# Performance work log

Measured on AMD Instinct MI355X. Metric: run time of the kernel, lower is better.

Reference implementation:

```python
import jax, jax.numpy as jnp
import numpy as np
import math

B, T, D, E, K, H = 2, 2048, 1024, 8, 2, 4096
CAP_F = 1.25
N = B * T
C = math.ceil(CAP_F * N * K / E)  # 1280


def setup_inputs() -> dict:
    key = jax.random.key(0)
    ks = jax.random.split(key, 4)
    s = 0.02
    return {
        "h": jax.random.normal(ks[0], (B, T, D), jnp.float32),
        "Wr": (jax.random.normal(ks[1], (D, E), jnp.float32) * s),
        "br": jnp.zeros((E,), jnp.float32),
        "ln_scale": jnp.ones((E, D), jnp.float32),
        "ln_bias": jnp.zeros((E, D), jnp.float32),
        "W1": (jax.random.normal(ks[2], (E, D, 2 * H), jnp.float32) * s),
        "b1": jnp.zeros((E, 2 * H), jnp.float32),
        "W2": (jax.random.normal(ks[3], (E, H, D), jnp.float32) * s),
        "b2": jnp.zeros((E, D), jnp.float32),
    }


def _cv_squared(x, eps=1e-9):
    m = x.mean()
    v = ((x - m) ** 2).mean()  # biased variance, as torch var(unbiased=False)
    return v / (jnp.maximum(m, eps) ** 2 + eps)


def reference(h, Wr, br, ln_scale, ln_bias, W1, b1, W2, b2):
    x = h.reshape(N, D)
    # ---- router (eval mode: no noise, temperature=1.0) ----
    logits = x @ Wr + br                                   # [N, E]
    z_loss = jnp.mean(logits ** 2) * 1e-4
    probs = jax.nn.softmax(logits, axis=-1)
    importance = probs.sum(0)                              # [E]
    topk_vals, topk_idx = jax.lax.top_k(logits, K)         # [N, K]
    gates = jax.nn.softmax(topk_vals, axis=-1)             # [N, K]

    # ---- capacity-limited positions, pass-major order (pass 0 all tokens, then pass 1) ----
    eid = topk_idx.T.reshape(-1)                           # [K*N] int
    onehot = jax.nn.one_hot(eid, E, dtype=jnp.int32)       # [K*N, E]
    pos = jnp.take_along_axis(jnp.cumsum(onehot, 0) - 1, eid[:, None], axis=1)[:, 0]
    keep = pos < C                                         # [K*N] bool
    load = jnp.sum(onehot * keep[:, None].astype(jnp.int32), axis=0).astype(jnp.float32)
    pos_c = jnp.minimum(pos, C - 1)
    nid = jnp.tile(jnp.arange(N), K)                       # token ids, pass-major

    # normalized combine weights per token (dropped slots get 0)
    keep_nk = keep.reshape(K, N).T                         # [N, K]
    kept_gates = gates * keep_nk.astype(gates.dtype)
    denom = jnp.maximum(kept_gates.sum(1, keepdims=True), 1e-8)
    w_flat = (kept_gates / denom).T.reshape(-1)            # [K*N], pass-major

    # ---- dispatch: scatter tokens into [E, C, D] (== einsum('nec,nd->ecd')) ----
    keep_f = keep[:, None].astype(x.dtype)
    expert_in = jnp.zeros((E, C, D), x.dtype).at[eid, pos_c].add(x[nid] * keep_f)

    # ---- experts: PreNorm + GLU FFN (dropout off in eval) ----
    mu = expert_in.mean(-1, keepdims=True)
    var = ((expert_in - mu) ** 2).mean(-1, keepdims=True)
    xn = (expert_in - mu) / jnp.sqrt(var + 1e-5)
    xn = xn * ln_scale[:, None, :] + ln_bias[:, None, :]
    u = jnp.einsum('ecd,edh->ech', xn, W1) + b1[:, None, :]  # [E, C, 2H]
    a, g = u[..., :H], u[..., H:]
    v = a * jax.nn.sigmoid(g)                               # GLU(dim=-1)
    expert_out = jnp.einsum('ech,ehd->ecd', v, W2) + b2[:, None, :]

    # ---- combine: gather expert slots, weight, scatter-add to tokens ----
    gathered = expert_out[eid, pos_c] * w_flat[:, None]
    y = jnp.zeros((N, D), x.dtype).at[nid].add(gathered).reshape(B, T, D)

    balance_loss = 0.5 * (_cv_squared(importance) + _cv_squared(load))
    return y, balance_loss, z_loss
```

## Files before the change

### kernel.cpp

```cpp
#include <hip/hip_runtime.h>
#include <cstdint>
#include <cstddef>

#define N_TOK 4096
#define DIM   1024
#define NEXP  8
#define HID   4096
#define TWO_H 8192
#define CAP   1280

typedef __bf16 bf16x8 __attribute__((ext_vector_type(8)));
typedef float  f32x4  __attribute__((ext_vector_type(4)));

__device__ __forceinline__ unsigned short f2bf(float f) {
  union { float f; unsigned u; } v; v.f = f;
  unsigned r = v.u + 0x7FFF + ((v.u >> 16) & 1);
  return (unsigned short)(r >> 16);
}
__device__ __forceinline__ float bf2f(unsigned short b) {
  union { unsigned u; float f; } v; v.u = ((unsigned)b) << 16;
  return v.f;
}

__global__ void k_zero(float* imp, float* zsum) {
  if (threadIdx.x < NEXP) imp[threadIdx.x] = 0.f;
  if (threadIdx.x == 0) zsum[0] = 0.f;
}

__global__ void k_conv_w1(const float* __restrict__ W1, unsigned short* __restrict__ W1t) {
  __shared__ float tA[32][33];
  __shared__ float tG[32][33];
  int h0 = blockIdx.x * 32, d0 = blockIdx.y * 32, e = blockIdx.z;
  int tx = threadIdx.x & 31, ty = threadIdx.x >> 5;
  const float* src = W1 + (size_t)e * DIM * TWO_H;
  for (int i = 0; i < 32; i += 8) {
    int d = d0 + ty + i;
    tA[ty + i][tx] = src[(size_t)d * TWO_H + h0 + tx];
    tG[ty + i][tx] = src[(size_t)d * TWO_H + HID + h0 + tx];
  }
  __syncthreads();
  unsigned short* dst = W1t + (size_t)e * TWO_H * DIM;
  for (int i = 0; i < 64; i += 8) {
    int r = ty + i;
    int hh = r >> 1, p = r & 1;
    float v = p ? tG[tx][hh] : tA[tx][hh];
    dst[(size_t)(2 * h0 + r) * DIM + d0 + tx] = f2bf(v);
  }
}

__global__ void k_conv_w2(const float* __restrict__ W2, unsigned short* __restrict__ W2t) {
  __shared__ float t[32][33];
  int d0 = blockIdx.x * 32, h0 = blockIdx.y * 32, e = blockIdx.z;
  int tx = threadIdx.x & 31, ty = threadIdx.x >> 5;
  const float* src = W2 + (size_t)e * HID * DIM;
  for (int i = 0; i < 32; i += 8)
    t[ty + i][tx] = src[(size_t)(h0 + ty + i) * DIM + d0 + tx];
  __syncthreads();
  unsigned short* dst = W2t + (size_t)e * DIM * HID;
  for (int i = 0; i < 32; i += 8)
    dst[(size_t)(d0 + ty + i) * HID + h0 + tx] = f2bf(t[tx][ty + i]);
}

__global__ void k_pack_b1(const float* __restrict__ b1, float* __restrict__ b1p) {
  int g = blockIdx.x * blockDim.x + threadIdx.x;
  int e = g >> 13, r = g & (TWO_H - 1);
  int h = r >> 1, p = r & 1;
  b1p[g] = b1[e * TWO_H + p * HID + h];
}

__global__ void __launch_bounds__(256) k_router(
    const float* __restrict__ x, const float* __restrict__ Wr, const float* __restrict__ br,
    int* __restrict__ idx, float* __restrict__ gate,
    float* __restrict__ imp, float* __restrict__ zsum) {
  __shared__ float sW[TWO_H];
  __shared__ float sX[16 * 1028];
  __shared__ float sLG[16 * 8];
  __shared__ float sImp[8];
  __shared__ float sZ;
  int tid = threadIdx.x;
  if (tid < 8) sImp[tid] = 0.f;
  if (tid == 8) sZ = 0.f;
  for (int i = 0; i < 8; ++i) {
    int g = tid + i * 256;
    *(float4*)&sW[g * 4] = *(const float4*)&Wr[g * 4];
  }
  int t0 = blockIdx.x * 16;
  const float* xb = x + (size_t)t0 * DIM;
  for (int i = 0; i < 16; ++i) {
    int g = tid + i * 256;
    int row = g >> 8, c = (g & 255) * 4;
    *(float4*)&sX[row * 1028 + c] = *(const float4*)&xb[(size_t)g * 4];
  }
  __syncthreads();
  int t = tid >> 4, e = (tid >> 1) & 7, half = tid & 1;
  const float* xr = &sX[t * 1028 + half * 512];
  float s = 0.f;
  for (int k = 0; k < 512; k += 4) {
    float4 xv = *(const float4*)&xr[k];
    int kb = (half * 512 + k) * 8 + e;
    s += xv.x * sW[kb] + xv.y * sW[kb + 8] + xv.z * sW[kb + 16] + xv.w * sW[kb + 24];
  }
  s += __shfl_xor(s, 1);
  if (half == 0) sLG[t * 8 + e] = s + br[e];
  __syncthreads();
  if (tid < 16) {
    int n = t0 + tid;
    float lg[8];
    for (int i = 0; i < 8; ++i) lg[i] = sLG[tid * 8 + i];
    float mx = lg[0];
    for (int i = 1; i < 8; ++i) mx = fmaxf(mx, lg[i]);
    float ex[8], den = 0.f, zs = 0.f;
    for (int i = 0; i < 8; ++i) { ex[i] = __expf(lg[i] - mx); den += ex[i]; zs += lg[i] * lg[i]; }
    atomicAdd(&sZ, zs);
    float rden = 1.f / den;
    for (int i = 0; i < 8; ++i) atomicAdd(&sImp[i], ex[i] * rden);
    int i1 = 0;
    for (int i = 1; i < 8; ++i) if (lg[i] > lg[i1]) i1 = i;
    int i2 = -1;
    for (int i = 0; i < 8; ++i) { if (i == i1) continue; if (i2 < 0 || lg[i] > lg[i2]) i2 = i; }
    float e2 = __expf(lg[i2] - lg[i1]);
    float g1 = 1.f / (1.f + e2);
    idx[n * 2] = i1; idx[n * 2 + 1] = i2;
    gate[n * 2] = g1; gate[n * 2 + 1] = 1.f - g1;
  }
  __syncthreads();
  if (tid < 8) atomicAdd(&imp[tid], sImp[tid]);
  if (tid == 8) atomicAdd(zsum, sZ);
}

__global__ void k_scan(const int* __restrict__ idx, int* __restrict__ pos, int* __restrict__ cnt) {
  int wave = threadIdx.x >> 6, lane = threadIdx.x & 63;
  int base = 0;
  for (int c = 0; c < (2 * N_TOK) / 64; ++c) {
    int s = c * 64 + lane;
    int n = s & (N_TOK - 1), k = s >> 12;
    int e = idx[n * 2 + k];
    unsigned long long m = __ballot(e == wave);
    if (e == wave) pos[s] = base + __popcll(m & ((1ull << lane) - 1ull));
    base += __popcll(m);
  }
  if (lane == 0) cnt[wave] = base;
}

__global__ void k_weights(const float* __restrict__ gate, const int* __restrict__ pos,
                          float* __restrict__ wn) {
  int n = blockIdx.x * blockDim.x + threadIdx.x;
  if (n >= N_TOK) return;
  float g0 = gate[n * 2], g1 = gate[n * 2 + 1];
  float k0 = (pos[n] < CAP) ? g0 : 0.f;
  float k1 = (pos[N_TOK + n] < CAP) ? g1 : 0.f;
  float den = fmaxf(k0 + k1, 1e-8f);
  wn[n * 2] = k0 / den; wn[n * 2 + 1] = k1 / den;
}

__global__ void __launch_bounds__(256) k_gather_ln(
    const float* __restrict__ x, const float* __restrict__ lns, const float* __restrict__ lnb,
    const int* __restrict__ idx, const int* __restrict__ pos, unsigned short* __restrict__ Xn) {
  int s = blockIdx.x;
  int p = pos[s];
  if (p >= CAP) return;
  int n = s & (N_TOK - 1), k = s >> 12;
  int e = idx[n * 2 + k];
  const float* xr = x + (size_t)n * DIM;
  int tid = threadIdx.x;
  float v[4], sum = 0.f, sq = 0.f;
  for (int i = 0; i < 4; ++i) { v[i] = xr[tid + i * 256]; sum += v[i]; sq += v[i] * v[i]; }
  for (int o = 32; o > 0; o >>= 1) { sum += __shfl_down(sum, o); sq += __shfl_down(sq, o); }
  __shared__ float ws[8];
  int wv = tid >> 6, ln = tid & 63;
  if (ln == 0) { ws[wv] = sum; ws[4 + wv] = sq; }
  __syncthreads();
  sum = ws[0] + ws[1] + ws[2] + ws[3];
  sq  = ws[4] + ws[5] + ws[6] + ws[7];
  float mu = sum * (1.f / DIM);
  float var = sq * (1.f / DIM) - mu * mu;
  float rs = rsqrtf(var + 1e-5f);
  unsigned short* orow = Xn + ((size_t)e * CAP + p) * DIM;
  const float* sc = lns + (size_t)e * DIM;
  const float* bi = lnb + (size_t)e * DIM;
  for (int i = 0; i < 4; ++i) {
    int d = tid + i * 256;
    orow[d] = f2bf((v[i] - mu) * rs * sc[d] + bi[d]);
  }
}

template<bool GLU>
__global__ void __launch_bounds__(256) k_gemm(
    const unsigned short* __restrict__ A,
    const unsigned short* __restrict__ B,
    const float* __restrict__ bias,
    unsigned short* __restrict__ Cout,
    int M, int Nn, int K) {
  __shared__ __align__(16) unsigned short smem[2 * 128 * 72];
  unsigned short* sA = smem;
  unsigned short* sB = smem + 128 * 72;
  int e  = blockIdx.z;
  int m0 = blockIdx.x * 128;
  int n0 = blockIdx.y * 128;
  const unsigned short* Ae = A + (size_t)e * M * K;
  const unsigned short* Be = B + (size_t)e * Nn * K;
  int tid = threadIdx.x;
  int lane = tid & 63, wave = tid >> 6;
  int wm = (wave >> 1) * 64, wn = (wave & 1) * 64;
  int quad = lane >> 4, l16 = lane & 15;
  f32x4 acc[4][4];
  for (int i = 0; i < 4; ++i)
    for (int j = 0; j < 4; ++j) acc[i][j] = f32x4{0.f, 0.f, 0.f, 0.f};

  int srow = tid >> 3;
  int schunk = (tid & 7) * 8;
  for (int k0 = 0; k0 < K; k0 += 64) {
    __syncthreads();
    for (int i = 0; i < 4; ++i) {
      int r = srow + i * 32;
      *(int4*)&sA[r * 72 + schunk] = *(const int4*)&Ae[(size_t)(m0 + r) * K + k0 + schunk];
      *(int4*)&sB[r * 72 + schunk] = *(const int4*)&Be[(size_t)(n0 + r) * K + k0 + schunk];
    }
    __syncthreads();
    for (int kk = 0; kk < 64; kk += 32) {
      bf16x8 aF[4], bF[4];
      for (int i = 0; i < 4; ++i) {
        aF[i] = *(const bf16x8*)&sA[(wm + i * 16 + l16) * 72 + kk + quad * 8];
        bF[i] = *(const bf16x8*)&sB[(wn + i * 16 + l16) * 72 + kk + quad * 8];
      }
      for (int i = 0; i < 4; ++i)
        for (int j = 0; j < 4; ++j)
          acc[i][j] = __builtin_amdgcn_mfma_f32_16x16x32_bf16(aF[i], bF[j], acc[i][j], 0, 0, 0);
    }
  }
  __syncthreads();
  if (GLU) {
    const float* bp = bias + (size_t)e * TWO_H;
    unsigned short* Ce = Cout + (size_t)e * M * (Nn >> 1);
    for (int i = 0; i < 4; ++i)
      for (int j = 0; j < 4; ++j) {
        int pn = n0 + wn + j * 16 + l16;
        float b = bp[pn];
        for (int r = 0; r < 4; ++r) {
          int row = wm + i * 16 + quad * 4 + r;
          float u = acc[i][j][r] + b;
          float g = __shfl_xor(u, 1);
          if ((l16 & 1) == 0) {
            float vv = u / (1.f + __expf(-g));
            smem[row * 80 + ((wn + j * 16 + l16) >> 1)] = f2bf(vv);
          }
        }
      }
    __syncthreads();
    int c = tid & 7, row0 = tid >> 3;
    for (int p = 0; p < 4; ++p) {
      int row = row0 + p * 32;
      *(int4*)&Ce[(size_t)(m0 + row) * (Nn >> 1) + (n0 >> 1) + c * 8] =
          *(const int4*)&smem[row * 80 + c * 8];
    }
  } else {
    unsigned short* Ce = Cout + (size_t)e * M * Nn;
    for (int i = 0; i < 4; ++i)
      for (int j = 0; j < 4; ++j) {
        int col = wn + j * 16 + l16;
        for (int r = 0; r < 4; ++r) {
          int row = wm + i * 16 + quad * 4 + r;
          smem[row * 136 + col] = f2bf(acc[i][j][r]);
        }
      }
    __syncthreads();
    int c = tid & 15, row0 = tid >> 4;
    for (int p = 0; p < 8; ++p) {
      int row = row0 + p * 16;
      *(int4*)&Ce[(size_t)(m0 + row) * Nn + n0 + c * 8] =
          *(const int4*)&smem[row * 136 + c * 8];
    }
  }
}

__global__ void __launch_bounds__(256) k_gather_out(
    const unsigned short* __restrict__ Yexp, const float* __restrict__ b2,
    const int* __restrict__ idx, const int* __restrict__ pos,
    const float* __restrict__ wn, float* __restrict__ y) {
  int n = blockIdx.x, tid = threadIdx.x;
  int e0 = idx[n * 2], e1 = idx[n * 2 + 1];
  int p0 = min(pos[n], CAP - 1), p1 = min(pos[N_TOK + n], CAP - 1);
  float w0 = wn[n * 2], w1 = wn[n * 2 + 1];
  const unsigned short* r0 = Yexp + ((size_t)e0 * CAP + p0) * DIM;
  const unsigned short* r1 = Yexp + ((size_t)e1 * CAP + p1) * DIM;
  const float* bb0 = b2 + (size_t)e0 * DIM;
  const float* bb1 = b2 + (size_t)e1 * DIM;
  float* yr = y + (size_t)n * DIM;
  for (int i = 0; i < 4; ++i) {
    int d = tid + i * 256;
    yr[d] = w0 * (bf2f(r0[d]) + bb0[d]) + w1 * (bf2f(r1[d]) + bb1[d]);
  }
}

__global__ void k_losses(const float* __restrict__ imp, const int* __restrict__ cnt,
                         const float* __restrict__ zsum, float* __restrict__ out) {
  if (threadIdx.x != 0 || blockIdx.x != 0) return;
  double li[8], ll[8], mi = 0.0, ml = 0.0;
  for (int i = 0; i < 8; ++i) {
    li[i] = imp[i];
    ll[i] = (double)min(cnt[i], CAP);
    mi += li[i]; ml += ll[i];
  }
  mi /= 8.0; ml /= 8.0;
  double vi = 0.0, vl = 0.0;
  for (int i = 0; i < 8; ++i) { vi += (li[i] - mi) * (li[i] - mi); vl += (ll[i] - ml) * (ll[i] - ml); }
  vi /= 8.0; vl /= 8.0;
  const double eps = 1e-9;
  double cvi = vi / (fmax(mi, eps) * fmax(mi, eps) + eps);
  double cvl = vl / (fmax(ml, eps) * fmax(ml, eps) + eps);
  out[0] = (float)(0.5 * (cvi + cvl));
  out[1] = (float)((double)zsum[0] / (double)(N_TOK * NEXP) * 1e-4);
}

extern "C" void kernel_launch(void* const* d_in, const int* in_sizes, int n_in,
                              void* d_out, int out_size, void* d_ws, size_t ws_size,
                              hipStream_t stream) {
  const float* h   = (const float*)d_in[0];
  const float* Wr  = (const float*)d_in[1];
  const float* br  = (const float*)d_in[2];
  const float* lns = (const float*)d_in[3];
  const float* lnb = (const float*)d_in[4];
  const float* W1  = (const float*)d_in[5];
  const float* b1  = (const float*)d_in[6];
  const float* W2  = (const float*)d_in[7];
  const float* b2  = (const float*)d_in[8];
  float* out = (float*)d_out;

  char* ws = (char*)d_ws;
  size_t off = 0;
  auto alloc = [&](size_t bytes) { char* p = ws + off; off += (bytes + 255) & ~(size_t)255; return p; };
  unsigned short* W1t = (unsigned short*)alloc((size_t)NEXP * TWO_H * DIM * 2);
  unsigned short* W2t = (unsigned short*)alloc((size_t)NEXP * DIM * HID * 2);
  unsigned short* Xn  = (unsigned short*)alloc((size_t)NEXP * CAP * DIM * 2);
  unsigned short* V   = (unsigned short*)alloc((size_t)NEXP * CAP * HID * 2);
  unsigned short* Yx  = (unsigned short*)alloc((size_t)NEXP * CAP * DIM * 2);
  float* b1p  = (float*)alloc((size_t)NEXP * TWO_H * 4);
  int*   idx  = (int*)alloc((size_t)N_TOK * 2 * 4);
  float* gate = (float*)alloc((size_t)N_TOK * 2 * 4);
  float* wn   = (float*)alloc((size_t)N_TOK * 2 * 4);
  int*   pos  = (int*)alloc((size_t)2 * N_TOK * 4);
  int*   cnt  = (int*)alloc(64);
  float* imp  = (float*)alloc(64);
  float* zsum = (float*)alloc(64);
  (void)ws_size; (void)in_sizes; (void)n_in; (void)out_size;

  k_zero<<<dim3(1), dim3(64), 0, stream>>>(imp, zsum);
  k_conv_w1<<<dim3(HID / 32, DIM / 32, NEXP), dim3(256), 0, stream>>>(W1, W1t);
  k_conv_w2<<<dim3(DIM / 32, HID / 32, NEXP), dim3(256), 0, stream>>>(W2, W2t);
  k_pack_b1<<<dim3(NEXP * TWO_H / 256), dim3(256), 0, stream>>>(b1, b1p);
  k_router<<<dim3(N_TOK / 16), dim3(256), 0, stream>>>(h, Wr, br, idx, gate, imp, zsum);
  k_scan<<<dim3(1), dim3(512), 0, stream>>>(idx, pos, cnt);
  k_weights<<<dim3(16), dim3(256), 0, stream>>>(gate, pos, wn);
  k_gather_ln<<<dim3(2 * N_TOK), dim3(256), 0, stream>>>(h, lns, lnb, idx, pos, Xn);
  k_gemm<true><<<dim3(CAP / 128, TWO_H / 128, NEXP), dim3(256), 0, stream>>>(
      Xn, W1t, b1p, V, CAP, TWO_H, DIM);
  k_gemm<false><<<dim3(CAP / 128, DIM / 128, NEXP), dim3(256), 0, stream>>>(
      V, W2t, b1p, Yx, CAP, DIM, HID);
  k_gather_out<<<dim3(N_TOK), dim3(256), 0, stream>>>(Yx, b2, idx, pos, wn, out);
  k_losses<<<dim3(1), dim3(64), 0, stream>>>(imp, cnt, zsum, out + (size_t)N_TOK * DIM);
}
```

Before: 1.069 ms.

## Use direct global-to-LDS loads and XCD-aware block remapping in expert GEMM

Replaces the register-staged global-to-shared tile copy with the global_load_lds builtin, which writes 16-byte chunks straight into LDS. The LDS row stride becomes an unpadded 64, matching the per-wave contiguous layout the builtin writes. Workgroup IDs are also remapped so consecutive logical tiles land on the same XCD for better L2 reuse. In exchange, dropping the padding may bring back LDS bank conflicts on the fragment reads, and the remap assumes the workgroup count divides by 8.

```diff
diff --git a/kernel.cpp b/kernel.cpp
--- a/kernel.cpp
+++ b/kernel.cpp
@@ -20,6 +20,12 @@
 __device__ __forceinline__ float bf2f(unsigned short b) {
   union { unsigned u; float f; } v; v.u = ((unsigned)b) << 16;
   return v.f;
+}
+
+__device__ __forceinline__ void gll16(const unsigned short* g, unsigned short* l) {
+  __builtin_amdgcn_global_load_lds(
+      (const __attribute__((address_space(1))) uint32_t*)g,
+      (__attribute__((address_space(3))) uint32_t*)l, 16, 0, 0);
 }
 
 __global__ void k_zero(float* imp, float* zsum) {
@@ -191,12 +197,18 @@
     const float* __restrict__ bias,
     unsigned short* __restrict__ Cout,
     int M, int Nn, int K) {
-  __shared__ __align__(16) unsigned short smem[2 * 128 * 72];
+  __shared__ __align__(16) unsigned short smem[17408];
   unsigned short* sA = smem;
-  unsigned short* sB = smem + 128 * 72;
-  int e  = blockIdx.z;
-  int m0 = blockIdx.x * 128;
-  int n0 = blockIdx.y * 128;
+  unsigned short* sB = smem + 128 * 64;
+
+  int gx = gridDim.x, gy = gridDim.y;
+  int nwg = gx * gy * (int)gridDim.z;
+  int bid = blockIdx.x + gx * (blockIdx.y + gy * blockIdx.z);
+  int lid = (bid & 7) * (nwg >> 3) + (bid >> 3);
+  int bm = lid % gx; int rest = lid / gx;
+  int e  = rest / gy;
+  int m0 = bm * 128, n0 = (rest % gy) * 128;
+
   const unsigned short* Ae = A + (size_t)e * M * K;
   const unsigned short* Be = B + (size_t)e * Nn * K;
   int tid = threadIdx.x;
@@ -207,21 +219,25 @@
   for (int i = 0; i < 4; ++i)
     for (int j = 0; j < 4; ++j) acc[i][j] = f32x4{0.f, 0.f, 0.f, 0.f};
 
-  int srow = tid >> 3;
-  int schunk = (tid & 7) * 8;
+  int srr = lane >> 3;
+  int scc = lane & 7;
+  const unsigned short* Ag = Ae + (size_t)(m0 + wave * 32 + srr) * K + scc * 8;
+  const unsigned short* Bg = Be + (size_t)(n0 + wave * 32 + srr) * K + scc * 8;
+  unsigned short* sAw = sA + wave * (32 * 64);
+  unsigned short* sBw = sB + wave * (32 * 64);
+
   for (int k0 = 0; k0 < K; k0 += 64) {
     __syncthreads();
-    for (int i = 0; i < 4; ++i) {
-      int r = srow + i * 32;
-      *(int4*)&sA[r * 72 + schunk] = *(const int4*)&Ae[(size_t)(m0 + r) * K + k0 + schunk];
-      *(int4*)&sB[r * 72 + schunk] = *(const int4*)&Be[(size_t)(n0 + r) * K + k0 + schunk];
+    for (int c = 0; c < 4; ++c) {
+      gll16(Ag + (size_t)(c * 8) * K + k0, sAw + c * (8 * 64));
+      gll16(Bg + (size_t)(c * 8) * K + k0, sBw + c * (8 * 64));
     }
     __syncthreads();
     for (int kk = 0; kk < 64; kk += 32) {
       bf16x8 aF[4], bF[4];
       for (int i = 0; i < 4; ++i) {
-        aF[i] = *(const bf16x8*)&sA[(wm + i * 16 + l16) * 72 + kk + quad * 8];
-        bF[i] = *(const bf16x8*)&sB[(wn + i * 16 + l16) * 72 + kk + quad * 8];
+        aF[i] = *(const bf16x8*)&sA[(wm + i * 16 + l16) * 64 + kk + quad * 8];
+        bF[i] = *(const bf16x8*)&sB[(wn + i * 16 + l16) * 64 + kk + quad * 8];
       }
       for (int i = 0; i < 4; ++i)
         for (int j = 0; j < 4; ++j)
```

Result: slower. 1.116 ms (+4.4%).
